# Kernel tuning notes

Hardware: AMD Instinct MI355X
Metric: run time of the kernel (lower is better)

Reference implementation:

```python
import jax, jax.numpy as jnp
import numpy as np

IMPOSSIBLE = -10000000.0
NUM_LABELS = 10
NUM_TAGS = 1 + 4 * NUM_LABELS  # 41
B, T = 4096, 256


def _bioul_constraints(num_labels):
    O, I, Bt, L, U = 0, 1, 2, 3, 4
    n = 1 + 4 * num_labels
    ft = np.ones((n, n), dtype=bool)
    ft[O, O] = False
    for i in range(num_labels):
        S = 4 * i
        for j in range(num_labels):
            SJ = 4 * j
            ft[L + S, Bt + SJ] = False
            ft[L + S, U + SJ] = False
            ft[U + S, Bt + SJ] = False
            ft[U + S, U + SJ] = False
        ft[O, Bt + S] = False
        ft[Bt + S, I + S] = False
        ft[I + S, I + S] = False
        ft[I + S, L + S] = False
        ft[Bt + S, L + S] = False
        ft[L + S, O] = False
        ft[O, U + S] = False
        ft[U + S, O] = False
    sft = np.zeros(n, dtype=bool)
    eft = np.zeros(n, dtype=bool)
    for i in range(num_labels):
        S = 4 * i
        sft[I + S] = True   # cannot start inside an entity
        sft[L + S] = True
        eft[I + S] = True   # cannot end inside an entity
        eft[Bt + S] = True
    return jnp.asarray(ft), jnp.asarray(sft), jnp.asarray(eft)


def setup_inputs() -> dict:
    key = jax.random.key(0)
    k1, k2, k3, k4, k5 = jax.random.split(key, 5)
    emissions = jax.random.normal(k1, (B, T, NUM_TAGS), dtype=jnp.float32)
    # left-aligned valid prefixes, as required by masked_flip semantics
    lengths = jax.random.randint(k2, (B,), T // 2, T + 1)
    mask = jnp.arange(T)[None, :] < lengths[:, None]
    # gold path: everything tagged O (tag 0) -- a valid BIOUL sequence
    target = jnp.zeros((B, T, NUM_TAGS), dtype=bool).at[:, :, 0].set(True)
    transitions = jax.random.normal(k3, (NUM_TAGS, NUM_TAGS), dtype=jnp.float32) * 0.1
    start_transitions = jax.random.normal(k4, (NUM_TAGS,), dtype=jnp.float32) * 0.1
    end_transitions = jax.random.normal(k5, (NUM_TAGS,), dtype=jnp.float32) * 0.1
    ft, sft, eft = _bioul_constraints(NUM_LABELS)
    return {
        "emissions": emissions,
        "mask": mask,
        "target": target,
        "transitions": transitions,
        "start_transitions": start_transitions,
        "end_transitions": end_transitions,
        "forbidden_transitions": ft,
        "start_forbidden_transitions": sft,
        "end_forbidden_transitions": eft,
    }


def _crf_loss(emissions, mask, target, transitions, start_transitions,
              end_transitions, ft, sft, eft):
    trans = jnp.where(ft, IMPOSSIBLE, transitions)           # [n, n]
    start = jnp.where(sft, IMPOSSIBLE, start_transitions)    # [n]
    end = jnp.where(eft, IMPOSSIBLE, end_transitions)        # [n]
    # supervised (target-restricted) and unsupervised emission scores
    sup = jnp.where(target, emissions, IMPOSSIBLE)           # [B, T, n]
    bi = jnp.stack([sup, emissions], axis=1)                 # [B, 2, T, n]
    bi = jnp.swapaxes(bi, 0, 2)                              # [T, 2, B, n]
    init = bi[0] + start                                     # [2, B, n]

    def step(prev, e_k):
        # logsumexp_reduce: alpha'[j] = logsumexp_i(alpha[i] + trans[i, j]) + e_k[j]
        nxt = jax.nn.logsumexp(prev[..., :, None] + trans, axis=-2) + e_k
        return nxt, nxt

    _, outs = jax.lax.scan(step, init, bi[1:])
    out = jnp.concatenate([init[None], outs], axis=0)        # [T, 2, B, n]
    out = jnp.swapaxes(out, 0, 2)                            # [B, 2, T, n]
    # masked_flip(...)[:, :, 0] == alpha at the last valid token
    lengths = mask.sum(-1)                                   # [B]
    idx = (lengths - 1)[:, None, None, None]
    z = jnp.take_along_axis(out, idx, axis=2)[:, :, 0] + end # [B, 2, n]
    supervised_z = jax.nn.logsumexp(z[:, 0], axis=-1)
    unsupervised_z = jax.nn.logsumexp(z[:, 1], axis=-1)
    return -(supervised_z - unsupervised_z)                  # [B]


def reference(emissions, mask, target, transitions, start_transitions,
              end_transitions, forbidden_transitions,
              start_forbidden_transitions, end_forbidden_transitions):
    return _crf_loss(emissions, mask, target, transitions, start_transitions,
                     end_transitions, forbidden_transitions,
                     start_forbidden_transitions, end_forbidden_transitions)
```

## Files before the change

kernel.cpp:

```cpp
#include <hip/hip_runtime.h>
#include <stdint.h>

#define NT 41
#define TT 256

typedef __attribute__((ext_vector_type(8))) short short8;
typedef __attribute__((ext_vector_type(16))) float f32x16;
typedef __attribute__((ext_vector_type(2))) int int2v;

union FragU { short8 s; uint32_t u[4]; };

static __device__ __forceinline__ uint32_t pk_bf16(float lo, float hi) {
    uint32_t d;
    asm("v_cvt_pk_bf16_f32 %0, %1, %2" : "=v"(d) : "v"(lo), "v"(hi));
    return d;
}
static __device__ __forceinline__ float asf(int x){ return __builtin_bit_cast(float, x); }
static __device__ __forceinline__ int   asi(float x){ return __builtin_bit_cast(int, x); }
static __device__ __forceinline__ float hsum(float x) {
    int2v r = __builtin_amdgcn_permlane32_swap(asi(x), asi(x), false, false);
    return asf(r[0]) + asf(r[1]);
}
static __device__ __forceinline__ uint32_t dpp_pairswap(uint32_t v) {
    return (uint32_t)__builtin_amdgcn_update_dpp(0, (int)v, 0xB1, 0xF, 0xF, true);
}
static __device__ __forceinline__ uint32_t u4c(uint4 v, int q) {
    return q==0 ? v.x : q==1 ? v.y : q==2 ? v.z : v.w;
}
static __device__ __forceinline__ short8 packB8(const float* g) {
    FragU u;
    u.u[0] = pk_bf16(g[0], g[1]); u.u[1] = pk_bf16(g[2], g[3]);
    u.u[2] = pk_bf16(g[4], g[5]); u.u[3] = pk_bf16(g[6], g[7]);
    return u.s;
}
static __device__ __forceinline__ short8 packTail(const float* g) {
    float tl[8] = {g[0], g[1], g[2], g[3], g[4], 0.f, 0.f, 0.f};
    return packB8(tl);
}
template<bool BYTE>
static __device__ __forceinline__ uint32_t bAt(const void* p, size_t idx) {
    if (BYTE) return (uint32_t)((const uint8_t*)p)[idx];
    return (((const uint32_t*)p)[idx] != 0u) ? 1u : 0u;
}
static __device__ __forceinline__ int rowOf(int rr, int h) {
    return (rr < 16) ? ((rr & 3) + 8 * (rr >> 2) + 4 * h)
                     : (32 + ((rr - 16) & 3) + 8 * ((rr - 16) >> 2) + 4 * h);
}
static __device__ __forceinline__ void mfma6(const short8* A, short8 B0, short8 B1, short8 B2,
                                             float* d ) {
    const f32x16 z16 = (f32x16)0.0f;
    f32x16 d0 = __builtin_amdgcn_mfma_f32_32x32x16_bf16(A[0], B0, z16, 0,0,0);
    d0 = __builtin_amdgcn_mfma_f32_32x32x16_bf16(A[1], B1, d0, 0,0,0);
    d0 = __builtin_amdgcn_mfma_f32_32x32x16_bf16(A[2], B2, d0, 0,0,0);
    f32x16 d1 = __builtin_amdgcn_mfma_f32_32x32x16_bf16(A[3], B0, z16, 0,0,0);
    d1 = __builtin_amdgcn_mfma_f32_32x32x16_bf16(A[4], B1, d1, 0,0,0);
    d1 = __builtin_amdgcn_mfma_f32_32x32x16_bf16(A[5], B2, d1, 0,0,0);
    #pragma unroll
    for (int rr = 0; rr < 16; ++rr) d[rr] = d0[rr];
    #pragma unroll
    for (int rr = 0; rr < 5; ++rr) d[16+rr] = d1[rr];
}

template<bool BYTE>
static __device__ void buildA(bool fwd, int c, int h, const float* trans,
                              const void* ftp, short8* A) {
    #pragma unroll
    for (int mb = 0; mb < 2; ++mb)
    #pragma unroll
    for (int ch = 0; ch < 3; ++ch) {
        float v[8];
        #pragma unroll
        for (int e = 0; e < 8; ++e) {
            const int src = (e&3) + 8*(e>>2) + 4*h + 16*ch;
            const int o = mb*32 + c;
            const int i_ = fwd ? src : o;
            const int j_ = fwd ? o : src;
            float val = 0.0f;
            if (src < NT && o < NT && bAt<BYTE>(ftp, i_*NT + j_) == 0u)
                val = __expf(trans[i_*NT + j_]);
            v[e] = val;
        }
        FragU u; u.u[0]=pk_bf16(v[0],v[1]); u.u[1]=pk_bf16(v[2],v[3]);
        u.u[2]=pk_bf16(v[4],v[5]); u.u[3]=pk_bf16(v[6],v[7]);
        A[mb*3 + ch] = u.s;
    }
}

template<bool BYTE, int N, bool ASC, bool PRE, bool REINIT>
static __device__ float run_pass(int t0, int len, bool sup, int h,
    const char* myrow, const float* emb, const uint8_t* tgb8,
    const short8* A, const float* endD, float aD[21])
{
    float w[3][21];
    uint4 S[3][5]; uint32_t S40[3];

    auto tAt = [&](int i){ return ASC ? (t0 + i) : (t0 - i); };
    auto issueSlot = [&](int sl, int t) {
        const char* rp = myrow + (size_t)t * (NT * 4);
        #pragma unroll
        for (int m = 0; m < 5; ++m) {
            const int off = 4 * ((m < 4) ? (8*m + 4*h) : (32 + 4*h));
            uint4 tmp; __builtin_memcpy(&tmp, rp + off, 16);
            S[sl][m] = tmp;
        }
        uint32_t t40; __builtin_memcpy(&t40, rp + 160, 4);
        S40[sl] = t40;
    };
    auto convSlot = [&](int sl) {
        #pragma unroll
        for (int rr = 0; rr < 21; ++rr) {
            uint32_t mine = (rr < 20) ? u4c(S[sl][rr>>2], rr & 3) : S40[sl];
            uint32_t oth = dpp_pairswap(mine);
            uint32_t embits = sup ? mine : oth;
            uint32_t tgbits = sup ? oth : mine;
            float e = __expf(__builtin_bit_cast(float, embits));
            w[sl][rr] = ((!sup) || (tgbits != 0u)) ? e : 0.0f;
        }
    };
    auto loadB = [&](int sl, int t) {
        const float* base = emb + (size_t)t * NT;
        const uint8_t* tb = tgb8 + (size_t)t * NT;
        const uint32_t om = sup ? 0u : 0x01010101u;
        float ev[21]; uint32_t tw[5]; uint32_t t40;
        #pragma unroll
        for (int m = 0; m < 5; ++m) {
            const int off = (m < 4) ? (8*m + 4*h) : (32 + 4*h);
            float4 tmp; __builtin_memcpy(&tmp, base + off, 16);
            ev[4*m+0]=tmp.x; ev[4*m+1]=tmp.y; ev[4*m+2]=tmp.z; ev[4*m+3]=tmp.w;
            uint32_t w_; __builtin_memcpy(&w_, tb + off, 4);
            tw[m] = w_ | om;
        }
        ev[20] = base[40];
        t40 = (((uint32_t)tb[40]) | om) & 0xffu;
        #pragma unroll
        for (int rr = 0; rr < 20; ++rr)
            w[sl][rr] = __expf(ev[rr]) * (float)((tw[rr>>2] >> (8*(rr&3))) & 0xffu);
        w[sl][20] = __expf(ev[20]) * (float)t40;
    };

    if (!BYTE) {
        issueSlot(0, tAt(0)); issueSlot(1, tAt(1)); issueSlot(2, tAt(2));
        convSlot(0);
    } else {
        loadB(0, tAt(0));
    }

    float logS = 0.0f;
    constexpr int NB3 = (N + 2) / 3;
    for (int bb = 0; bb < NB3; ++bb) {
        #pragma unroll
        for (int s = 0; s < 3; ++s) {
            const int i = bb * 3 + s;
            if (i < N) {
                if (!BYTE) { if (i + 3 < N) issueSlot(s, tAt(i + 3)); }
                const int t = tAt(i);
                short8 B0, B1, B2;
                if (PRE) {
                    float tmp[21];
                    #pragma unroll
                    for (int rr = 0; rr < 21; ++rr) tmp[rr] = aD[rr] * w[s][rr];
                    B0 = packB8(tmp); B1 = packB8(tmp+8); B2 = packTail(tmp+16);
                } else {
                    B0 = packB8(aD); B1 = packB8(aD+8); B2 = packTail(aD+16);
                }
                float d[21]; mfma6(A, B0, B1, B2, d);
                if (PRE) {
                    #pragma unroll
                    for (int rr = 0; rr < 21; ++rr) aD[rr] = d[rr];
                } else if (REINIT) {
                    const bool sel = (len - 1 == t);
                    #pragma unroll
                    for (int rr = 0; rr < 21; ++rr)
                        aD[rr] = (sel ? endD[rr] : d[rr]) * w[s][rr];
                } else {
                    #pragma unroll
                    for (int rr = 0; rr < 21; ++rr) aD[rr] = d[rr] * w[s][rr];
                }
                if ((t & 7) == 0) {
                    const bool started = (!REINIT) || (len - 1 >= t);
                    float cs = 0.0f;
                    #pragma unroll
                    for (int rr = 0; rr < 21; ++rr) cs += aD[rr];
                    cs = hsum(cs);
                    const float csc = fmaxf(cs, 1e-30f);
                    const float rinv = started ? (1.0f / csc) : 1.0f;
                    logS += started ? __logf(csc) : 0.0f;
                    #pragma unroll
                    for (int rr = 0; rr < 21; ++rr) aD[rr] *= rinv;
                }
                if (i + 1 < N) {
                    if (BYTE) loadB((s + 1) % 3, tAt(i + 1));
                    else      convSlot((s + 1) % 3);
                }
            }
        }
    }
    return logS;
}

template<bool BYTE>
static __device__ void run_all(const float* __restrict__ em, const void* __restrict__ maskp,
    const void* __restrict__ tgtp, const float* __restrict__ trans,
    const float* __restrict__ st, const float* __restrict__ en,
    const void* __restrict__ ftp, const void* __restrict__ sftp,
    const void* __restrict__ eftp, float* __restrict__ out)
{
    __shared__ float sb[6][21][64];
    __shared__ float ssig[6][64];

    const int tid  = threadIdx.x;
    const int wid  = tid >> 6;
    const int lane = tid & 63;
    const int c = lane & 31;
    const int h = lane >> 5;
    const int bbase = blockIdx.x * 16;
    const int b = bbase + (c >> 1);
    const bool sup = ((c & 1) == 0);
    const size_t eb0 = (size_t)b * TT * NT;

    int len = 0;
    if (BYTE) {
        const uint8_t* mr = (const uint8_t*)maskp + (size_t)b * TT;
        #pragma unroll
        for (int k = 0; k < 16; ++k) {
            uint4 v; __builtin_memcpy(&v, mr + k*16, 16);
            len += __popc(v.x)+__popc(v.y)+__popc(v.z)+__popc(v.w);
        }
    } else {
        const uint32_t* mr = (const uint32_t*)maskp + (size_t)b * TT;
        for (int k = 0; k < TT; k += 4) {
            uint4 v; __builtin_memcpy(&v, mr + k, 16);
            len += (v.x!=0)+(v.y!=0)+(v.z!=0)+(v.w!=0);
        }
    }

    const char* myrow = sup ? (const char*)(em + eb0)
                            : (const char*)tgtp + eb0 * 4;
    const float*  emb  = em + eb0;
    const uint8_t* tgb8 = (const uint8_t*)tgtp + eb0;

    const bool isFwdA = (wid == 0 || wid == 1 || wid == 5);
    short8 A[6];
    buildA<BYTE>(isFwdA, c, h, trans, ftp, A);

    float endD[21];
    if (wid == 3 || wid == 4) {
        #pragma unroll
        for (int rr = 0; rr < 21; ++rr) {
            const int row = rowOf(rr, h);
            endD[rr] = (row < NT && bAt<BYTE>(eftp, row) == 0u) ? __expf(en[row]) : 0.0f;
        }
    }

    float aD[21];
    float sig = 0.0f;

    if (wid == 0) {
        #pragma unroll
        for (int rr = 0; rr < 21; ++rr) {
            const int row = rowOf(rr, h);
            float val = 0.0f;
            if (row < NT) {
                float wv = __expf(em[eb0 + row]);
                if (sup) wv *= (bAt<BYTE>(tgtp, eb0 + row) ? 1.0f : 0.0f);
                const float se = (bAt<BYTE>(sftp, row) == 0u) ? __expf(st[row]) : 0.0f;
                val = wv * se;
            }
            aD[rr] = val;
        }
        sig = run_pass<BYTE,63,true,false,false>(1, len, sup, h, myrow, emb, tgb8, A, endD, aD);
    } else if (wid == 1) {
        #pragma unroll
        for (int rr = 0; rr < 21; ++rr) aD[rr] = (rowOf(rr,h) < NT) ? 1.0f : 0.0f;
        sig = run_pass<BYTE,64,true,false,false>(64, len, sup, h, myrow, emb, tgb8, A, endD, aD);
    } else if (wid == 2) {
        #pragma unroll
        for (int rr = 0; rr < 21; ++rr) aD[rr] = (rowOf(rr,h) < NT) ? 1.0f : 0.0f;
        sig = run_pass<BYTE,64,false,true,false>(127, len, sup, h, myrow, emb, tgb8, A, endD, aD);
    } else if (wid == 3) {
        #pragma unroll
        for (int rr = 0; rr < 21; ++rr) aD[rr] = 0.0f;
        sig = run_pass<BYTE,64,false,false,true>(255, len, sup, h, myrow, emb, tgb8, A, endD, aD);
    } else if (wid == 4) {
        #pragma unroll
        for (int rr = 0; rr < 21; ++rr) aD[rr] = (rowOf(rr,h) < NT) ? 1.0f : 0.0f;
        sig = run_pass<BYTE,64,false,false,true>(191, len, sup, h, myrow, emb, tgb8, A, endD, aD);
    } else {
        #pragma unroll
        for (int rr = 0; rr < 21; ++rr) aD[rr] = (rowOf(rr,h) < NT) ? 1.0f : 0.0f;
        sig = run_pass<BYTE,64,true,true,false>(128, len, sup, h, myrow, emb, tgb8, A, endD, aD);
    }

    #pragma unroll
    for (int rr = 0; rr < 21; ++rr) sb[wid][rr][lane] = aD[rr];
    ssig[wid][lane] = sig;

    __syncthreads();

    if (wid == 0) {
        float endC[21];
        #pragma unroll
        for (int rr = 0; rr < 21; ++rr) {
            const int row = rowOf(rr, h);
            endC[rr] = (row < NT && bAt<BYTE>(eftp, row) == 0u) ? __expf(en[row]) : 0.0f;
        }
        float yB[21], g4[21];
        float d1=0.f, d2=0.f, d3=0.f, d4=0.f, d5e=0.f;
        #pragma unroll
        for (int rr = 0; rr < 21; ++rr) {
            const int row = rowOf(rr, h);
            const float uv = (row < NT) ? 1.0f : 0.0f;
            const float a63 = sb[0][rr][lane];
            const float zB  = sb[2][rr][lane];
            yB[rr]          = sb[1][rr][lane];
            const float g9  = sb[3][rr][lane];
            g4[rr]          = sb[4][rr][lane];
            const float z2  = sb[5][rr][lane];
            d1 += zB * a63; d2 += yB[rr] * uv; d3 += z2 * g9;
            d4 += g4[rr] * uv; d5e += yB[rr] * endC[rr];
        }
        d1 = hsum(d1); d2 = hsum(d2); d3 = hsum(d3); d4 = hsum(d4); d5e = hsum(d5e);

        short8 B0 = packB8(yB), B1 = packB8(yB+8), B2 = packTail(yB+16);
        float ey[21]; mfma6(A, B0, B1, B2, ey);
        float d5 = 0.f;
        #pragma unroll
        for (int rr = 0; rr < 21; ++rr) d5 += ey[rr] * g4[rr];
        d5 = hsum(d5);

        const float sA = ssig[0][lane], szv = ssig[2][lane];
        const float s3 = ssig[3][lane], s4 = ssig[4][lane], s5 = ssig[5][lane];
        const float base = szv + sA + __logf(fmaxf(d1, 1e-37f)) - __logf(fmaxf(d2, 1e-37f));
        const float l5  = __logf(fmaxf(d5, 1e-37f));
        const float tail =
            (len == 128) ? __logf(fmaxf(d5e, 1e-37f))
          : (len <= 192) ? (l5 + s4)
          : (l5 + s3 + s5 + __logf(fmaxf(d3, 1e-37f)) - __logf(fmaxf(d4, 1e-37f)));
        const float zc = base + tail;
        const float zo = __shfl_xor(zc, 1);
        if ((lane & 1) == 0 && lane < 32)
            out[bbase + (lane >> 1)] = zo - zc;
    }
}

__global__ __launch_bounds__(384) void crf_seg(
    const float* __restrict__ em, const void* __restrict__ maskp,
    const void* __restrict__ tgtp, const float* __restrict__ trans,
    const float* __restrict__ st, const float* __restrict__ en,
    const void* __restrict__ ftp, const void* __restrict__ sftp,
    const void* __restrict__ eftp, float* __restrict__ out)
{
    const bool byteMode = (*(const uint32_t*)maskp == 0x01010101u);
    if (byteMode) run_all<true >(em, maskp, tgtp, trans, st, en, ftp, sftp, eftp, out);
    else          run_all<false>(em, maskp, tgtp, trans, st, en, ftp, sftp, eftp, out);
}

extern "C" void kernel_launch(void* const* d_in, const int* in_sizes, int n_in,
                              void* d_out, int out_size, void* d_ws, size_t ws_size,
                              hipStream_t stream) {
    const float* em    = (const float*)d_in[0];
    const void*  maskp = d_in[1];
    const void*  tgtp  = d_in[2];
    const float* trans = (const float*)d_in[3];
    const float* st    = (const float*)d_in[4];
    const float* en    = (const float*)d_in[5];
    const void*  ftp   = d_in[6];
    const void*  sftp  = d_in[7];
    const void*  eftp  = d_in[8];
    float* out = (float*)d_out;

    crf_seg<<<4096 / 16, 384, 0, stream>>>(em, maskp, tgtp, trans, st, en,
                                           ftp, sftp, eftp, out);
}
```

Measured before the change: 136.0 us.

## Split CRF time scan into 32-step segments across 14 waves

The sequential forward recursion is split into eight 32-step time segments instead of four 64-step ones, handled by 14 wavefronts per block instead of 6. Partial transfer products are combined at the end with more dot products and logs, keyed on which segment holds the last valid token. The goal is to shorten the serial dependency chain per wave. The cost is more redundant work, more LDS, and a 896-thread block limited to one block per CU by the launch bounds.

```diff
diff --git a/kernel.cpp b/kernel.cpp
--- a/kernel.cpp
+++ b/kernel.cpp
@@ -177,13 +177,13 @@
                     for (int rr = 0; rr < 21; ++rr) aD[rr] = d[rr] * w[s][rr];
                 }
                 if ((t & 7) == 0) {
-                    const bool started = (!REINIT) || (len - 1 >= t);
                     float cs = 0.0f;
                     #pragma unroll
                     for (int rr = 0; rr < 21; ++rr) cs += aD[rr];
                     cs = hsum(cs);
                     const float csc = fmaxf(cs, 1e-30f);
-                    const float rinv = started ? (1.0f / csc) : 1.0f;
+                    const float rinv = 1.0f / csc;
+                    const bool started = (!REINIT) || (len - 1 >= t);
                     logS += started ? __logf(csc) : 0.0f;
                     #pragma unroll
                     for (int rr = 0; rr < 21; ++rr) aD[rr] *= rinv;
@@ -205,8 +205,8 @@
     const void* __restrict__ ftp, const void* __restrict__ sftp,
     const void* __restrict__ eftp, float* __restrict__ out)
 {
-    __shared__ float sb[6][21][64];
-    __shared__ float ssig[6][64];
+    __shared__ float sb[14][21][64];
+    __shared__ float ssig[14][64];
 
     const int tid  = threadIdx.x;
     const int wid  = tid >> 6;
@@ -239,12 +239,12 @@
     const float*  emb  = em + eb0;
     const uint8_t* tgb8 = (const uint8_t*)tgtp + eb0;
 
-    const bool isFwdA = (wid == 0 || wid == 1 || wid == 5);
+    const bool isFwdA = (wid <= 3) || (wid >= 11);
     short8 A[6];
     buildA<BYTE>(isFwdA, c, h, trans, ftp, A);
 
     float endD[21];
-    if (wid == 3 || wid == 4) {
+    if (wid >= 7 && wid <= 10) {
         #pragma unroll
         for (int rr = 0; rr < 21; ++rr) {
             const int row = rowOf(rr, h);
@@ -268,27 +268,19 @@
             }
             aD[rr] = val;
         }
-        sig = run_pass<BYTE,63,true,false,false>(1, len, sup, h, myrow, emb, tgb8, A, endD, aD);
-    } else if (wid == 1) {
+        sig = run_pass<BYTE,31,true,false,false>(1, len, sup, h, myrow, emb, tgb8, A, endD, aD);
+    } else {
         #pragma unroll
         for (int rr = 0; rr < 21; ++rr) aD[rr] = (rowOf(rr,h) < NT) ? 1.0f : 0.0f;
-        sig = run_pass<BYTE,64,true,false,false>(64, len, sup, h, myrow, emb, tgb8, A, endD, aD);
-    } else if (wid == 2) {
-        #pragma unroll
-        for (int rr = 0; rr < 21; ++rr) aD[rr] = (rowOf(rr,h) < NT) ? 1.0f : 0.0f;
-        sig = run_pass<BYTE,64,false,true,false>(127, len, sup, h, myrow, emb, tgb8, A, endD, aD);
-    } else if (wid == 3) {
-        #pragma unroll
-        for (int rr = 0; rr < 21; ++rr) aD[rr] = 0.0f;
-        sig = run_pass<BYTE,64,false,false,true>(255, len, sup, h, myrow, emb, tgb8, A, endD, aD);
-    } else if (wid == 4) {
-        #pragma unroll
-        for (int rr = 0; rr < 21; ++rr) aD[rr] = (rowOf(rr,h) < NT) ? 1.0f : 0.0f;
-        sig = run_pass<BYTE,64,false,false,true>(191, len, sup, h, myrow, emb, tgb8, A, endD, aD);
-    } else {
-        #pragma unroll
-        for (int rr = 0; rr < 21; ++rr) aD[rr] = (rowOf(rr,h) < NT) ? 1.0f : 0.0f;
-        sig = run_pass<BYTE,64,true,true,false>(128, len, sup, h, myrow, emb, tgb8, A, endD, aD);
+        if (wid <= 3) {
+            sig = run_pass<BYTE,32,true,false,false>(32*wid, len, sup, h, myrow, emb, tgb8, A, endD, aD);
+        } else if (wid <= 6) {
+            sig = run_pass<BYTE,32,false,true,false>(32*(wid-3)+31, len, sup, h, myrow, emb, tgb8, A, endD, aD);
+        } else if (wid <= 10) {
+            sig = run_pass<BYTE,32,false,false,true>(32*(wid-3)+31, len, sup, h, myrow, emb, tgb8, A, endD, aD);
+        } else {
+            sig = run_pass<BYTE,32,true,true,false>(32*(wid-7), len, sup, h, myrow, emb, tgb8, A, endD, aD);
+        }
     }
 
     #pragma unroll
@@ -298,52 +290,71 @@
     __syncthreads();
 
     if (wid == 0) {
-        float endC[21];
+        float endC[21], uD[21];
         #pragma unroll
         for (int rr = 0; rr < 21; ++rr) {
             const int row = rowOf(rr, h);
             endC[rr] = (row < NT && bAt<BYTE>(eftp, row) == 0u) ? __expf(en[row]) : 0.0f;
-        }
-        float yB[21], g4[21];
-        float d1=0.f, d2=0.f, d3=0.f, d4=0.f, d5e=0.f;
-        #pragma unroll
-        for (int rr = 0; rr < 21; ++rr) {
-            const int row = rowOf(rr, h);
-            const float uv = (row < NT) ? 1.0f : 0.0f;
-            const float a63 = sb[0][rr][lane];
-            const float zB  = sb[2][rr][lane];
-            yB[rr]          = sb[1][rr][lane];
-            const float g9  = sb[3][rr][lane];
-            g4[rr]          = sb[4][rr][lane];
-            const float z2  = sb[5][rr][lane];
-            d1 += zB * a63; d2 += yB[rr] * uv; d3 += z2 * g9;
-            d4 += g4[rr] * uv; d5e += yB[rr] * endC[rr];
-        }
-        d1 = hsum(d1); d2 = hsum(d2); d3 = hsum(d3); d4 = hsum(d4); d5e = hsum(d5e);
-
-        short8 B0 = packB8(yB), B1 = packB8(yB+8), B2 = packTail(yB+16);
-        float ey[21]; mfma6(A, B0, B1, B2, ey);
-        float d5 = 0.f;
-        #pragma unroll
-        for (int rr = 0; rr < 21; ++rr) d5 += ey[rr] * g4[rr];
-        d5 = hsum(d5);
-
-        const float sA = ssig[0][lane], szv = ssig[2][lane];
-        const float s3 = ssig[3][lane], s4 = ssig[4][lane], s5 = ssig[5][lane];
-        const float base = szv + sA + __logf(fmaxf(d1, 1e-37f)) - __logf(fmaxf(d2, 1e-37f));
-        const float l5  = __logf(fmaxf(d5, 1e-37f));
-        const float tail =
-            (len == 128) ? __logf(fmaxf(d5e, 1e-37f))
-          : (len <= 192) ? (l5 + s4)
-          : (l5 + s3 + s5 + __logf(fmaxf(d3, 1e-37f)) - __logf(fmaxf(d4, 1e-37f)));
-        const float zc = base + tail;
+            uD[rr] = (row < NT) ? 1.0f : 0.0f;
+        }
+        float dA=0.f,n1=0.f,d12=0.f,n2=0.f,d23=0.f,n3=0.f,dBe=0.f;
+        float y3v[21];
+        #pragma unroll
+        for (int rr = 0; rr < 21; ++rr) {
+            const float p0v = aD[rr];
+            const float y1 = sb[1][rr][lane], y2 = sb[2][rr][lane];
+            y3v[rr] = sb[3][rr][lane];
+            dA  += sb[4][rr][lane] * p0v;
+            d12 += sb[5][rr][lane] * y1;
+            d23 += sb[6][rr][lane] * y2;
+            n1  += y1 * uD[rr]; n2 += y2 * uD[rr]; n3 += y3v[rr] * uD[rr];
+            dBe += y3v[rr] * endC[rr];
+        }
+        dA=hsum(dA); n1=hsum(n1); d12=hsum(d12); n2=hsum(n2);
+        d23=hsum(d23); n3=hsum(n3); dBe=hsum(dBe);
+
+        short8 B0 = packB8(y3v), B1 = packB8(y3v+8), B2 = packTail(y3v+16);
+        float Bv[21]; mfma6(A, B0, B1, B2, Bv);
+
+        float t4=0.f,n4=0.f,t45=0.f,n5=0.f,t56=0.f,n6=0.f,t67=0.f;
+        #pragma unroll
+        for (int rr = 0; rr < 21; ++rr) {
+            const float g4 = sb[7][rr][lane], g5 = sb[8][rr][lane];
+            const float g6 = sb[9][rr][lane], g7 = sb[10][rr][lane];
+            t4  += Bv[rr] * g4;              n4 += uD[rr] * g4;
+            t45 += sb[11][rr][lane] * g5;    n5 += uD[rr] * g5;
+            t56 += sb[12][rr][lane] * g6;    n6 += uD[rr] * g6;
+            t67 += sb[13][rr][lane] * g7;
+        }
+        t4=hsum(t4); n4=hsum(n4); t45=hsum(t45); n5=hsum(n5);
+        t56=hsum(t56); n6=hsum(n6); t67=hsum(t67);
+
+        auto lg = [](float x){ return __logf(fmaxf(x, 1e-37f)); };
+        const float s0  = ssig[0][lane];
+        const float sz1 = ssig[4][lane], sz2 = ssig[5][lane], sz3 = ssig[6][lane];
+        const float sG4 = ssig[7][lane], sG5 = ssig[8][lane];
+        const float sG6 = ssig[9][lane], sG7 = ssig[10][lane];
+        const float sZ4 = ssig[11][lane], sZ5 = ssig[12][lane], sZ6 = ssig[13][lane];
+
+        const float L_low = s0 + sz1 + sz2 + sz3
+                          + lg(dA) - lg(n1) + lg(d12) - lg(n2) + lg(d23) - lg(n3);
+        const int m = (len - 1) >> 5;
+        float tail;
+        if (m == 3)      tail = lg(dBe);
+        else if (m == 4) tail = lg(t4) + sG4;
+        else if (m == 5) tail = lg(t4) - lg(n4) + lg(t45) + sZ4 + sG5;
+        else if (m == 6) tail = lg(t4) - lg(n4) + lg(t45) - lg(n5) + lg(t56)
+                               + sZ4 + sZ5 + sG6;
+        else             tail = lg(t4) - lg(n4) + lg(t45) - lg(n5) + lg(t56) - lg(n6)
+                               + lg(t67) + sZ4 + sZ5 + sZ6 + sG7;
+        const float zc = L_low + tail;
         const float zo = __shfl_xor(zc, 1);
         if ((lane & 1) == 0 && lane < 32)
             out[bbase + (lane >> 1)] = zo - zc;
     }
 }
 
-__global__ __launch_bounds__(384) void crf_seg(
+__global__ __launch_bounds__(896, 1) void crf_seg8(
     const float* __restrict__ em, const void* __restrict__ maskp,
     const void* __restrict__ tgtp, const float* __restrict__ trans,
     const float* __restrict__ st, const float* __restrict__ en,
@@ -369,6 +380,6 @@
     const void*  eftp  = d_in[8];
     float* out = (float*)d_out;
 
-    crf_seg<<<4096 / 16, 384, 0, stream>>>(em, maskp, tgtp, trans, st, en,
-                                           ftp, sftp, eftp, out);
-}
+    crf_seg8<<<4096 / 16, 896, 0, stream>>>(em, maskp, tgtp, trans, st, en,
+                                            ftp, sftp, eftp, out);
+}
```

Measured after the change: 514.3 us. 278% more time.
